# Kernel tuning notes

Measured on AMD Instinct MI355X. Metric: run time of the kernel, lower is better.

## Reference

```python
import jax, jax.numpy as jnp
import numpy as np

N_NODES = 30000
IN_DIM = 8
HIDDEN = 64
HEADS1 = 8
OUT_DIM = 8
NEG_SLOPE = 0.2


def _glorot(key, shape):
    fan_in, fan_out = shape[0], shape[-1]
    lim = jnp.sqrt(6.0 / (fan_in + fan_out))
    return jax.random.uniform(key, shape, jnp.float32, -lim, lim)


def setup_inputs() -> dict:
    key = jax.random.key(0)
    ks = jax.random.split(key, 12)
    x = jax.random.normal(ks[0], (N_NODES, IN_DIM), jnp.float32)
    edge_index = jax.random.randint(ks[1], (2, 300000), 0, N_NODES, jnp.int32)
    # layer 1: in=8, out=HIDDEN per head, 8 heads, concat
    W1l = _glorot(ks[2], (IN_DIM, HEADS1 * HIDDEN))
    W1r = _glorot(ks[3], (IN_DIM, HEADS1 * HIDDEN))
    a1 = _glorot(ks[4], (HEADS1, HIDDEN))
    b1 = jnp.zeros((HEADS1 * HIDDEN,), jnp.float32)
    # layer 2: in=HEADS1*HIDDEN, out=OUT_DIM, 1 head
    W2l = _glorot(ks[5], (HEADS1 * HIDDEN, OUT_DIM))
    W2r = _glorot(ks[6], (HEADS1 * HIDDEN, OUT_DIM))
    a2 = _glorot(ks[7], (1, OUT_DIM))
    b2 = jnp.zeros((OUT_DIM,), jnp.float32)
    return {"x": x, "edge_index": edge_index, "W1l": W1l, "W1r": W1r,
            "a1": a1, "b1": b1, "W2l": W2l, "W2r": W2r, "a2": a2, "b2": b2}


def gatv2_layer(x, src, dst, Wl, Wr, att, bias, heads, out_ch):
    n = x.shape[0]
    xl = (x @ Wl).reshape(n, heads, out_ch)   # messages (source side)
    xr = (x @ Wr).reshape(n, heads, out_ch)   # target side
    h = jax.nn.leaky_relu(xl[src] + xr[dst], NEG_SLOPE)   # [E,H,C]
    e = jnp.einsum('ehc,hc->eh', h, att)                  # [E,H]
    # segment softmax over incoming edges per destination node
    m = jax.ops.segment_max(e, dst, num_segments=n)
    p = jnp.exp(e - m[dst])
    denom = jax.ops.segment_sum(p, dst, num_segments=n)
    alpha = p / denom[dst]                                # [E,H]
    out = jax.ops.segment_sum(alpha[..., None] * xl[src], dst, num_segments=n)
    return out.reshape(n, heads * out_ch) + bias


def reference(x, edge_index, W1l, W1r, a1, b1, W2l, W2r, a2, b2):
    n = x.shape[0]
    loops = jnp.arange(n, dtype=edge_index.dtype)
    src = jnp.concatenate([edge_index[0], loops])  # add_self_loops=True (PyG default)
    dst = jnp.concatenate([edge_index[1], loops])
    h = gatv2_layer(x, src, dst, W1l, W1r, a1, b1, HEADS1, HIDDEN)
    h = jax.nn.relu(h)
    out = gatv2_layer(h, src, dst, W2l, W2r, a2, b2, 1, OUT_DIM)
    return out
```

## Files before the change

### kernel.cpp

```cpp
#include <hip/hip_runtime.h>
#include <math.h>

#define N_NODES   30000
#define N_EDGE    300000
#define N_EDGE_T  330000
#define HEADS     8
#define HIDDEN    64
#define IN_DIM    8
#define OUT_DIM   8
#define NEG_SLOPE 0.2f

#define PIN_V(v) asm volatile("" : "+v"(v))

#define DPP_ADDF(x, ctrl)                                                     \
    x += __int_as_float(__builtin_amdgcn_update_dpp(                          \
            0, __float_as_int(x), (ctrl), 0xF, 0xF, true))
#define RED16(x) do { DPP_ADDF(x, 0xB1); DPP_ADDF(x, 0x4E);                   \
                      DPP_ADDF(x, 0x141); DPP_ADDF(x, 0x140); } while (0)
#define RED8(x)  do { DPP_ADDF(x, 0xB1); DPP_ADDF(x, 0x4E);                   \
                      DPP_ADDF(x, 0x141); } while (0)


__global__ __launch_bounds__(256) void zero_kernel(int* __restrict__ count) {
    int i = blockIdx.x * 256 + threadIdx.x;
    if (i < N_NODES) count[i] = 0;
}

__global__ __launch_bounds__(256) void count_kernel(const int* __restrict__ ei,
                                                    int* __restrict__ count) {
    int e = blockIdx.x * 256 + threadIdx.x;
    if (e >= N_EDGE_T) return;
    int d = (e < N_EDGE) ? ei[N_EDGE + e] : (e - N_EDGE);
    atomicAdd(&count[d], 1);
}

__global__ __launch_bounds__(1024) void scan_kernel(const int* __restrict__ count,
                                                    int* __restrict__ row_start,
                                                    int* __restrict__ cursor) {
    __shared__ int wsum[16];
    const int tid  = threadIdx.x;
    const int wave = tid >> 6;
    const int lane = tid & 63;
    const int4* c4 = (const int4*)count;
    const int N4 = N_NODES / 4;
    int run = 0;
    for (int r = 0; r < 4; ++r) {
        const int g  = r * 1024 + tid;
        const int i0 = 2 * g;
        const int i1 = 2 * g + 1;
        int4 v0 = make_int4(0,0,0,0), v1 = make_int4(0,0,0,0);
        if (i0 < N4) v0 = c4[i0];
        if (i1 < N4) v1 = c4[i1];
        int s = v0.x + v0.y + v0.z + v0.w + v1.x + v1.y + v1.z + v1.w;
        int sc = s;
        #pragma unroll
        for (int off = 1; off < 64; off <<= 1) {
            int t = __shfl_up(sc, off, 64);
            if (lane >= off) sc += t;
        }
        if (lane == 63) wsum[wave] = sc;
        __syncthreads();
        if (tid < 16) {
            int w = wsum[tid];
            #pragma unroll
            for (int off = 1; off < 16; off <<= 1) {
                int t = __shfl_up(w, off, 64);
                if (tid >= off) w += t;
            }
            wsum[tid] = w;
        }
        __syncthreads();
        const int woff = (wave > 0) ? wsum[wave - 1] : 0;
        int e0 = run + woff + (sc - s);
        int4 ex0, ex1;
        ex0.x = e0;           ex0.y = ex0.x + v0.x;
        ex0.z = ex0.y + v0.y; ex0.w = ex0.z + v0.z;
        int e4 = ex0.w + v0.w;
        ex1.x = e4;           ex1.y = ex1.x + v1.x;
        ex1.z = ex1.y + v1.y; ex1.w = ex1.z + v1.z;
        if (i0 < N4) { ((int4*)row_start)[i0] = ex0; ((int4*)cursor)[i0] = ex0; }
        if (i1 < N4) { ((int4*)row_start)[i1] = ex1; ((int4*)cursor)[i1] = ex1; }
        const int tot = wsum[15];
        __syncthreads();
        run += tot;
    }
    if (tid == 0) row_start[N_NODES] = run;
}

__global__ __launch_bounds__(256) void scatter_kernel(const int* __restrict__ ei,
                                                      int* __restrict__ cursor,
                                                      int* __restrict__ edge_src) {
    int e = blockIdx.x * 256 + threadIdx.x;
    if (e >= N_EDGE_T) return;
    int s, d;
    if (e < N_EDGE) { s = ei[e]; d = ei[N_EDGE + e]; }
    else            { s = d = e - N_EDGE; }
    int pos = atomicAdd(&cursor[d], 1);
    edge_src[pos] = s;
}


__device__ __forceinline__ float4 ld_row4(const float* __restrict__ x, int s, int o) {
    return *(const float4*)(x + s * IN_DIM + o);
}

__global__ void __launch_bounds__(128, 3)
layer1_kernel(
    const float* __restrict__ x,
    const float* __restrict__ W1l, const float* __restrict__ W1r,
    const float* __restrict__ a1,  const float* __restrict__ b1,
    const float* __restrict__ W2l, const float* __restrict__ W2r,
    const int* __restrict__ row_start, const int* __restrict__ edge_src,
    float* __restrict__ xl2, float* __restrict__ xr2)
{
    const int d    = blockIdx.x;
    const int tid  = threadIdx.x;
    const int head = tid >> 4;
    const int c4   = tid & 15;
    const int colb = head * HIDDEN + c4 * 4;

    int vz; asm("v_mov_b32 %0, 0" : "=v"(vz));
    const int* __restrict__ es = edge_src + vz;

    float wl[IN_DIM][4], av[4];
    #pragma unroll
    for (int k = 0; k < IN_DIM; ++k) {
        const float4 l4 = *(const float4*)&W1l[k * 512 + colb];
        wl[k][0] = l4.x; wl[k][1] = l4.y; wl[k][2] = l4.z; wl[k][3] = l4.w;
    }
    { const float4 a4 = *(const float4*)&a1[colb];
      av[0] = a4.x; av[1] = a4.y; av[2] = a4.z; av[3] = a4.w; }

    float xr[4] = {0.f, 0.f, 0.f, 0.f};
    #pragma unroll
    for (int k = 0; k < IN_DIM; ++k) {
        const float4 r4 = *(const float4*)&W1r[k * 512 + colb];
        const float xv = x[d * IN_DIM + k];
        xr[0] = fmaf(xv, r4.x, xr[0]); xr[1] = fmaf(xv, r4.y, xr[1]);
        xr[2] = fmaf(xv, r4.z, xr[2]); xr[3] = fmaf(xv, r4.w, xr[3]);
    }

    #pragma unroll
    for (int k = 0; k < IN_DIM; ++k) {
        PIN_V(wl[k][0]); PIN_V(wl[k][1]); PIN_V(wl[k][2]); PIN_V(wl[k][3]);
    }
    PIN_V(av[0]); PIN_V(av[1]); PIN_V(av[2]); PIN_V(av[3]);
    PIN_V(xr[0]); PIN_V(xr[1]); PIN_V(xr[2]); PIN_V(xr[3]);

    const int rs = row_start[d];
    const int re = row_start[d + 1];

    float denom  = 0.f;
    float acc[4] = {0.f, 0.f, 0.f, 0.f};

    auto pair2 = [&](float4 a0, float4 a1_, float4 b0, float4 b1_,
                     bool va, bool vb) {
        const float ra[IN_DIM] = {a0.x, a0.y, a0.z, a0.w, a1_.x, a1_.y, a1_.z, a1_.w};
        const float rb[IN_DIM] = {b0.x, b0.y, b0.z, b0.w, b1_.x, b1_.y, b1_.z, b1_.w};
        float v0a = xr[0], v1a = xr[1], v2a = xr[2], v3a = xr[3];
        float v0b = xr[0], v1b = xr[1], v2b = xr[2], v3b = xr[3];
        #pragma unroll
        for (int k = 0; k < IN_DIM; ++k) {
            const float xa = ra[k], xb = rb[k];
            v0a = fmaf(xa, wl[k][0], v0a); v0b = fmaf(xb, wl[k][0], v0b);
            v1a = fmaf(xa, wl[k][1], v1a); v1b = fmaf(xb, wl[k][1], v1b);
            v2a = fmaf(xa, wl[k][2], v2a); v2b = fmaf(xb, wl[k][2], v2b);
            v3a = fmaf(xa, wl[k][3], v3a); v3b = fmaf(xb, wl[k][3], v3b);
        }
        float ta, tb, ea, eb;
        ta = fmaxf(v0a, NEG_SLOPE * v0a); ea = av[0] * ta;
        tb = fmaxf(v0b, NEG_SLOPE * v0b); eb = av[0] * tb;
        ta = fmaxf(v1a, NEG_SLOPE * v1a); ea = fmaf(av[1], ta, ea);
        tb = fmaxf(v1b, NEG_SLOPE * v1b); eb = fmaf(av[1], tb, eb);
        ta = fmaxf(v2a, NEG_SLOPE * v2a); ea = fmaf(av[2], ta, ea);
        tb = fmaxf(v2b, NEG_SLOPE * v2b); eb = fmaf(av[2], tb, eb);
        ta = fmaxf(v3a, NEG_SLOPE * v3a); ea = fmaf(av[3], ta, ea);
        tb = fmaxf(v3b, NEG_SLOPE * v3b); eb = fmaf(av[3], tb, eb);
        RED16(ea); RED16(eb);
        float pa = va ? __expf(ea) : 0.f;
        float pb = vb ? __expf(eb) : 0.f;
        denom += pa + pb;
        acc[0] = fmaf(pb, v0b, fmaf(pa, v0a, acc[0]));
        acc[1] = fmaf(pb, v1b, fmaf(pa, v1a, acc[1]));
        acc[2] = fmaf(pb, v2b, fmaf(pa, v2a, acc[2]));
        acc[3] = fmaf(pb, v3b, fmaf(pa, v3a, acc[3]));
    };

    float4 rA0, rA1, rB0, rB1, rC0, rC1, rD0, rD1;
    {
        int e1 = (rs + 1 < re) ? rs + 1 : re - 1;
        int e2 = (rs + 2 < re) ? rs + 2 : re - 1;
        int e3 = (rs + 3 < re) ? rs + 3 : re - 1;
        int s0 = es[rs], s1 = es[e1], s2 = es[e2], s3 = es[e3];
        rA0 = ld_row4(x, s0, 0); rA1 = ld_row4(x, s0, 4);
        rB0 = ld_row4(x, s1, 0); rB1 = ld_row4(x, s1, 4);
        rC0 = ld_row4(x, s2, 0); rC1 = ld_row4(x, s2, 4);
        rD0 = ld_row4(x, s3, 0); rD1 = ld_row4(x, s3, 4);
    }

    int base = rs;
    for (;;) {
        const int  nbase = base + 4;
        const bool more  = nbase < re;

        int ns0 = 0, ns1 = 0, ns2 = 0, ns3 = 0;
        if (more) {
            int f1 = (nbase + 1 < re) ? nbase + 1 : re - 1;
            int f2 = (nbase + 2 < re) ? nbase + 2 : re - 1;
            int f3 = (nbase + 3 < re) ? nbase + 3 : re - 1;
            ns0 = es[nbase]; ns1 = es[f1]; ns2 = es[f2]; ns3 = es[f3];
        }

        pair2(rA0, rA1, rB0, rB1, true, base + 1 < re);

        float4 nA0, nA1, nB0, nB1, nC0, nC1, nD0, nD1;
        if (more) {
            nA0 = ld_row4(x, ns0, 0); nA1 = ld_row4(x, ns0, 4);
            nB0 = ld_row4(x, ns1, 0); nB1 = ld_row4(x, ns1, 4);
            nC0 = ld_row4(x, ns2, 0); nC1 = ld_row4(x, ns2, 4);
            nD0 = ld_row4(x, ns3, 0); nD1 = ld_row4(x, ns3, 4);
        }

        pair2(rC0, rC1, rD0, rD1, base + 2 < re, base + 3 < re);

        if (!more) break;
        base = nbase;
        rA0 = nA0; rA1 = nA1; rB0 = nB0; rB1 = nB1;
        rC0 = nC0; rC1 = nC1; rD0 = nD0; rD1 = nD1;
    }

    const float inv = 1.f / denom;
    const float4 b4 = *(const float4*)&b1[colb];
    float hv[4];
    hv[0] = fmaxf(fmaf(acc[0], inv, b4.x - xr[0]), 0.f);
    hv[1] = fmaxf(fmaf(acc[1], inv, b4.y - xr[1]), 0.f);
    hv[2] = fmaxf(fmaf(acc[2], inv, b4.z - xr[2]), 0.f);
    hv[3] = fmaxf(fmaf(acc[3], inv, b4.w - xr[3]), 0.f);

    float vl[OUT_DIM], vr[OUT_DIM];
    #pragma unroll
    for (int j = 0; j < OUT_DIM; ++j) { vl[j] = 0.f; vr[j] = 0.f; }
    #pragma unroll
    for (int i = 0; i < 4; ++i) {
        const float4 l0 = *(const float4*)&W2l[(colb + i) * OUT_DIM];
        const float4 l1 = *(const float4*)&W2l[(colb + i) * OUT_DIM + 4];
        const float4 r0 = *(const float4*)&W2r[(colb + i) * OUT_DIM];
        const float4 r1 = *(const float4*)&W2r[(colb + i) * OUT_DIM + 4];
        vl[0] = fmaf(hv[i], l0.x, vl[0]); vl[1] = fmaf(hv[i], l0.y, vl[1]);
        vl[2] = fmaf(hv[i], l0.z, vl[2]); vl[3] = fmaf(hv[i], l0.w, vl[3]);
        vl[4] = fmaf(hv[i], l1.x, vl[4]); vl[5] = fmaf(hv[i], l1.y, vl[5]);
        vl[6] = fmaf(hv[i], l1.z, vl[6]); vl[7] = fmaf(hv[i], l1.w, vl[7]);
        vr[0] = fmaf(hv[i], r0.x, vr[0]); vr[1] = fmaf(hv[i], r0.y, vr[1]);
        vr[2] = fmaf(hv[i], r0.z, vr[2]); vr[3] = fmaf(hv[i], r0.w, vr[3]);
        vr[4] = fmaf(hv[i], r1.x, vr[4]); vr[5] = fmaf(hv[i], r1.y, vr[5]);
        vr[6] = fmaf(hv[i], r1.z, vr[6]); vr[7] = fmaf(hv[i], r1.w, vr[7]);
    }
    #pragma unroll
    for (int j = 0; j < OUT_DIM; ++j) { RED16(vl[j]); RED16(vr[j]); }

    __shared__ float psl[HEADS][OUT_DIM];
    __shared__ float psr[HEADS][OUT_DIM];
    if (c4 == 0) {
        #pragma unroll
        for (int j = 0; j < OUT_DIM; ++j) { psl[head][j] = vl[j]; psr[head][j] = vr[j]; }
    }
    __syncthreads();
    if (tid < 16) {
        const int side = tid >> 3, j = tid & 7;
        float s = 0.f;
        if (side == 0) {
            #pragma unroll
            for (int h = 0; h < HEADS; ++h) s += psl[h][j];
            xl2[d * OUT_DIM + j] = s;
        } else {
            #pragma unroll
            for (int h = 0; h < HEADS; ++h) s += psr[h][j];
            xr2[d * OUT_DIM + j] = s;
        }
    }
}


__global__ __launch_bounds__(256) void layer2_kernel(
    const float* __restrict__ xl2, const float* __restrict__ xr2,
    const float* __restrict__ a2,  const float* __restrict__ b2,
    const int* __restrict__ row_start, const int* __restrict__ edge_src,
    float* __restrict__ out)
{
    const int wave = threadIdx.x >> 6;
    const int lane = threadIdx.x & 63;
    const int d = blockIdx.x * 4 + wave;
    if (d >= N_NODES) return;
    const int sub = lane >> 3;
    const int c   = lane & 7;

    const float a_c  = a2[c];
    const float xr_d = xr2[d * OUT_DIM + c];

    const int rs = row_start[d];
    const int re = row_start[d + 1];

    float denom = 0.f, acc = 0.f;

    for (int base = rs; base < re; base += 8) {
        int e = base + sub;
        bool valid = (e < re);
        int s = valid ? edge_src[e] : 0;
        float xls = xl2[s * OUT_DIM + c];
        float v = xls + xr_d;
        float t = fmaxf(v, NEG_SLOPE * v);
        float eh = a_c * t;
        RED8(eh);
        float p = valid ? __expf(eh) : 0.f;
        denom += p;
        acc = fmaf(p, xls, acc);
    }

    denom += __shfl_xor(denom, 8,  64);  acc += __shfl_xor(acc, 8,  64);
    denom += __shfl_xor(denom, 16, 64);  acc += __shfl_xor(acc, 16, 64);
    denom += __shfl_xor(denom, 32, 64);  acc += __shfl_xor(acc, 32, 64);

    if (sub == 0) out[d * OUT_DIM + c] = acc / denom + b2[c];
}


extern "C" void kernel_launch(void* const* d_in, const int* in_sizes, int n_in,
                              void* d_out, int out_size, void* d_ws, size_t ws_size,
                              hipStream_t stream) {
    const float* x   = (const float*)d_in[0];
    const int*   ei  = (const int*)  d_in[1];
    const float* W1l = (const float*)d_in[2];
    const float* W1r = (const float*)d_in[3];
    const float* a1  = (const float*)d_in[4];
    const float* b1  = (const float*)d_in[5];
    const float* W2l = (const float*)d_in[6];
    const float* W2r = (const float*)d_in[7];
    const float* a2  = (const float*)d_in[8];
    const float* b2  = (const float*)d_in[9];
    float* out = (float*)d_out;

    char* ws = (char*)d_ws;
    size_t off = 0;
    auto carve = [&](size_t bytes) { char* p = ws + off; off += (bytes + 255) & ~size_t(255); return p; };
    int*   count     = (int*)  carve(N_NODES * sizeof(int));
    int*   row_start = (int*)  carve((N_NODES + 1) * sizeof(int));
    int*   cursor    = (int*)  carve(N_NODES * sizeof(int));
    int*   edge_src  = (int*)  carve(N_EDGE_T * sizeof(int));
    float* xl2       = (float*)carve(N_NODES * OUT_DIM * sizeof(float));
    float* xr2       = (float*)carve(N_NODES * OUT_DIM * sizeof(float));

    zero_kernel   <<<(N_NODES  + 255) / 256, 256, 0, stream>>>(count);
    count_kernel  <<<(N_EDGE_T + 255) / 256, 256, 0, stream>>>(ei, count);
    scan_kernel   <<<1, 1024, 0, stream>>>(count, row_start, cursor);
    scatter_kernel<<<(N_EDGE_T + 255) / 256, 256, 0, stream>>>(ei, cursor, edge_src);
    layer1_kernel <<<N_NODES, 128, 0, stream>>>(x, W1l, W1r, a1, b1, W2l, W2r,
                                                row_start, edge_src, xl2, xr2);
    layer2_kernel <<<(N_NODES + 3) / 4, 256, 0, stream>>>(xl2, xr2, a2, b2,
                                                          row_start, edge_src, out);
}
```

Baseline: 307.0 us.

## Precompute layer-1 source projection table instead of recomputing per edge

Adds a projection kernel that materialises xl = x @ W1l for all nodes (30000x512 floats), and layer1 now gathers 16-byte slices of this table per edge rather than gathering 32-byte x rows and doing 32 FMAs per edge. This removes per-edge recomputation and frees the registers that held W1l, so the occupancy hint rises from 3 to 4. In exchange it writes and then randomly reads a table of roughly 61 MB, so per-edge gather traffic grows from one 32-byte x row to the full 2 KB table row across the 128 threads, which may not stay in cache.

```diff
diff --git a/kernel.cpp b/kernel.cpp
--- a/kernel.cpp
+++ b/kernel.cpp
@@ -100,14 +100,37 @@
 }
 
 
-__device__ __forceinline__ float4 ld_row4(const float* __restrict__ x, int s, int o) {
-    return *(const float4*)(x + s * IN_DIM + o);
-}
-
-__global__ void __launch_bounds__(128, 3)
+__global__ __launch_bounds__(256) void proj_kernel(
+    const float* __restrict__ x, const float* __restrict__ W1l,
+    float* __restrict__ xl_t)
+{
+    const int t = threadIdx.x;
+    float wl0[IN_DIM], wl1[IN_DIM];
+    #pragma unroll
+    for (int k = 0; k < IN_DIM; ++k) {
+        wl0[k] = W1l[k * 512 + t];
+        wl1[k] = W1l[k * 512 + t + 256];
+    }
+    for (int n = blockIdx.x; n < N_NODES; n += gridDim.x) {
+        float xv[IN_DIM];
+        #pragma unroll
+        for (int k = 0; k < IN_DIM; ++k) xv[k] = x[n * IN_DIM + k];
+        float l0 = 0.f, l1 = 0.f;
+        #pragma unroll
+        for (int k = 0; k < IN_DIM; ++k) {
+            l0 = fmaf(xv[k], wl0[k], l0);
+            l1 = fmaf(xv[k], wl1[k], l1);
+        }
+        xl_t[n * 512 + t]       = l0;
+        xl_t[n * 512 + t + 256] = l1;
+    }
+}
+
+
+__global__ void __launch_bounds__(128, 4)
 layer1_kernel(
     const float* __restrict__ x,
-    const float* __restrict__ W1l, const float* __restrict__ W1r,
+    const float* __restrict__ xl_t, const float* __restrict__ W1r,
     const float* __restrict__ a1,  const float* __restrict__ b1,
     const float* __restrict__ W2l, const float* __restrict__ W2r,
     const int* __restrict__ row_start, const int* __restrict__ edge_src,
@@ -119,33 +142,20 @@
     const int c4   = tid & 15;
     const int colb = head * HIDDEN + c4 * 4;
 
-    int vz; asm("v_mov_b32 %0, 0" : "=v"(vz));
-    const int* __restrict__ es = edge_src + vz;
-
-    float wl[IN_DIM][4], av[4];
-    #pragma unroll
-    for (int k = 0; k < IN_DIM; ++k) {
-        const float4 l4 = *(const float4*)&W1l[k * 512 + colb];
-        wl[k][0] = l4.x; wl[k][1] = l4.y; wl[k][2] = l4.z; wl[k][3] = l4.w;
-    }
+    float av[4];
     { const float4 a4 = *(const float4*)&a1[colb];
       av[0] = a4.x; av[1] = a4.y; av[2] = a4.z; av[3] = a4.w; }
 
-    float xr[4] = {0.f, 0.f, 0.f, 0.f};
+    float xrv[4] = {0.f, 0.f, 0.f, 0.f};
     #pragma unroll
     for (int k = 0; k < IN_DIM; ++k) {
         const float4 r4 = *(const float4*)&W1r[k * 512 + colb];
         const float xv = x[d * IN_DIM + k];
-        xr[0] = fmaf(xv, r4.x, xr[0]); xr[1] = fmaf(xv, r4.y, xr[1]);
-        xr[2] = fmaf(xv, r4.z, xr[2]); xr[3] = fmaf(xv, r4.w, xr[3]);
-    }
-
-    #pragma unroll
-    for (int k = 0; k < IN_DIM; ++k) {
-        PIN_V(wl[k][0]); PIN_V(wl[k][1]); PIN_V(wl[k][2]); PIN_V(wl[k][3]);
+        xrv[0] = fmaf(xv, r4.x, xrv[0]); xrv[1] = fmaf(xv, r4.y, xrv[1]);
+        xrv[2] = fmaf(xv, r4.z, xrv[2]); xrv[3] = fmaf(xv, r4.w, xrv[3]);
     }
     PIN_V(av[0]); PIN_V(av[1]); PIN_V(av[2]); PIN_V(av[3]);
-    PIN_V(xr[0]); PIN_V(xr[1]); PIN_V(xr[2]); PIN_V(xr[3]);
+    PIN_V(xrv[0]); PIN_V(xrv[1]); PIN_V(xrv[2]); PIN_V(xrv[3]);
 
     const int rs = row_start[d];
     const int re = row_start[d + 1];
@@ -153,49 +163,40 @@
     float denom  = 0.f;
     float acc[4] = {0.f, 0.f, 0.f, 0.f};
 
-    auto pair2 = [&](float4 a0, float4 a1_, float4 b0, float4 b1_,
-                     bool va, bool vb) {
-        const float ra[IN_DIM] = {a0.x, a0.y, a0.z, a0.w, a1_.x, a1_.y, a1_.z, a1_.w};
-        const float rb[IN_DIM] = {b0.x, b0.y, b0.z, b0.w, b1_.x, b1_.y, b1_.z, b1_.w};
-        float v0a = xr[0], v1a = xr[1], v2a = xr[2], v3a = xr[3];
-        float v0b = xr[0], v1b = xr[1], v2b = xr[2], v3b = xr[3];
-        #pragma unroll
-        for (int k = 0; k < IN_DIM; ++k) {
-            const float xa = ra[k], xb = rb[k];
-            v0a = fmaf(xa, wl[k][0], v0a); v0b = fmaf(xb, wl[k][0], v0b);
-            v1a = fmaf(xa, wl[k][1], v1a); v1b = fmaf(xb, wl[k][1], v1b);
-            v2a = fmaf(xa, wl[k][2], v2a); v2b = fmaf(xb, wl[k][2], v2b);
-            v3a = fmaf(xa, wl[k][3], v3a); v3b = fmaf(xb, wl[k][3], v3b);
-        }
+    auto ldrow = [&](int s) { return *(const float4*)&xl_t[s * 512 + colb]; };
+
+    auto pair2 = [&](float4 ra, float4 rb, bool va, bool vb) {
+        float q0a = ra.x + xrv[0], q1a = ra.y + xrv[1];
+        float q2a = ra.z + xrv[2], q3a = ra.w + xrv[3];
+        float q0b = rb.x + xrv[0], q1b = rb.y + xrv[1];
+        float q2b = rb.z + xrv[2], q3b = rb.w + xrv[3];
         float ta, tb, ea, eb;
-        ta = fmaxf(v0a, NEG_SLOPE * v0a); ea = av[0] * ta;
-        tb = fmaxf(v0b, NEG_SLOPE * v0b); eb = av[0] * tb;
-        ta = fmaxf(v1a, NEG_SLOPE * v1a); ea = fmaf(av[1], ta, ea);
-        tb = fmaxf(v1b, NEG_SLOPE * v1b); eb = fmaf(av[1], tb, eb);
-        ta = fmaxf(v2a, NEG_SLOPE * v2a); ea = fmaf(av[2], ta, ea);
-        tb = fmaxf(v2b, NEG_SLOPE * v2b); eb = fmaf(av[2], tb, eb);
-        ta = fmaxf(v3a, NEG_SLOPE * v3a); ea = fmaf(av[3], ta, ea);
-        tb = fmaxf(v3b, NEG_SLOPE * v3b); eb = fmaf(av[3], tb, eb);
+        ta = fmaxf(q0a, NEG_SLOPE * q0a); ea = av[0] * ta;
+        tb = fmaxf(q0b, NEG_SLOPE * q0b); eb = av[0] * tb;
+        ta = fmaxf(q1a, NEG_SLOPE * q1a); ea = fmaf(av[1], ta, ea);
+        tb = fmaxf(q1b, NEG_SLOPE * q1b); eb = fmaf(av[1], tb, eb);
+        ta = fmaxf(q2a, NEG_SLOPE * q2a); ea = fmaf(av[2], ta, ea);
+        tb = fmaxf(q2b, NEG_SLOPE * q2b); eb = fmaf(av[2], tb, eb);
+        ta = fmaxf(q3a, NEG_SLOPE * q3a); ea = fmaf(av[3], ta, ea);
+        tb = fmaxf(q3b, NEG_SLOPE * q3b); eb = fmaf(av[3], tb, eb);
         RED16(ea); RED16(eb);
         float pa = va ? __expf(ea) : 0.f;
         float pb = vb ? __expf(eb) : 0.f;
         denom += pa + pb;
-        acc[0] = fmaf(pb, v0b, fmaf(pa, v0a, acc[0]));
-        acc[1] = fmaf(pb, v1b, fmaf(pa, v1a, acc[1]));
-        acc[2] = fmaf(pb, v2b, fmaf(pa, v2a, acc[2]));
-        acc[3] = fmaf(pb, v3b, fmaf(pa, v3a, acc[3]));
+        acc[0] = fmaf(pb, rb.x, fmaf(pa, ra.x, acc[0]));
+        acc[1] = fmaf(pb, rb.y, fmaf(pa, ra.y, acc[1]));
+        acc[2] = fmaf(pb, rb.z, fmaf(pa, ra.z, acc[2]));
+        acc[3] = fmaf(pb, rb.w, fmaf(pa, ra.w, acc[3]));
     };
 
-    float4 rA0, rA1, rB0, rB1, rC0, rC1, rD0, rD1;
+    float4 rA, rB, rC, rD;
     {
         int e1 = (rs + 1 < re) ? rs + 1 : re - 1;
         int e2 = (rs + 2 < re) ? rs + 2 : re - 1;
         int e3 = (rs + 3 < re) ? rs + 3 : re - 1;
-        int s0 = es[rs], s1 = es[e1], s2 = es[e2], s3 = es[e3];
-        rA0 = ld_row4(x, s0, 0); rA1 = ld_row4(x, s0, 4);
-        rB0 = ld_row4(x, s1, 0); rB1 = ld_row4(x, s1, 4);
-        rC0 = ld_row4(x, s2, 0); rC1 = ld_row4(x, s2, 4);
-        rD0 = ld_row4(x, s3, 0); rD1 = ld_row4(x, s3, 4);
+        int s0 = edge_src[rs], s1 = edge_src[e1];
+        int s2 = edge_src[e2], s3 = edge_src[e3];
+        rA = ldrow(s0); rB = ldrow(s1); rC = ldrow(s2); rD = ldrow(s3);
     }
 
     int base = rs;
@@ -208,34 +209,31 @@
             int f1 = (nbase + 1 < re) ? nbase + 1 : re - 1;
             int f2 = (nbase + 2 < re) ? nbase + 2 : re - 1;
             int f3 = (nbase + 3 < re) ? nbase + 3 : re - 1;
-            ns0 = es[nbase]; ns1 = es[f1]; ns2 = es[f2]; ns3 = es[f3];
-        }
-
-        pair2(rA0, rA1, rB0, rB1, true, base + 1 < re);
-
-        float4 nA0, nA1, nB0, nB1, nC0, nC1, nD0, nD1;
+            ns0 = edge_src[nbase]; ns1 = edge_src[f1];
+            ns2 = edge_src[f2];    ns3 = edge_src[f3];
+        }
+
+        pair2(rA, rB, true, base + 1 < re);
+
+        float4 nA, nB, nC, nD;
         if (more) {
-            nA0 = ld_row4(x, ns0, 0); nA1 = ld_row4(x, ns0, 4);
-            nB0 = ld_row4(x, ns1, 0); nB1 = ld_row4(x, ns1, 4);
-            nC0 = ld_row4(x, ns2, 0); nC1 = ld_row4(x, ns2, 4);
-            nD0 = ld_row4(x, ns3, 0); nD1 = ld_row4(x, ns3, 4);
-        }
-
-        pair2(rC0, rC1, rD0, rD1, base + 2 < re, base + 3 < re);
+            nA = ldrow(ns0); nB = ldrow(ns1); nC = ldrow(ns2); nD = ldrow(ns3);
+        }
+
+        pair2(rC, rD, base + 2 < re, base + 3 < re);
 
         if (!more) break;
         base = nbase;
-        rA0 = nA0; rA1 = nA1; rB0 = nB0; rB1 = nB1;
-        rC0 = nC0; rC1 = nC1; rD0 = nD0; rD1 = nD1;
+        rA = nA; rB = nB; rC = nC; rD = nD;
     }
 
     const float inv = 1.f / denom;
     const float4 b4 = *(const float4*)&b1[colb];
     float hv[4];
-    hv[0] = fmaxf(fmaf(acc[0], inv, b4.x - xr[0]), 0.f);
-    hv[1] = fmaxf(fmaf(acc[1], inv, b4.y - xr[1]), 0.f);
-    hv[2] = fmaxf(fmaf(acc[2], inv, b4.z - xr[2]), 0.f);
-    hv[3] = fmaxf(fmaf(acc[3], inv, b4.w - xr[3]), 0.f);
+    hv[0] = fmaxf(fmaf(acc[0], inv, b4.x), 0.f);
+    hv[1] = fmaxf(fmaf(acc[1], inv, b4.y), 0.f);
+    hv[2] = fmaxf(fmaf(acc[2], inv, b4.z), 0.f);
+    hv[3] = fmaxf(fmaf(acc[3], inv, b4.w), 0.f);
 
     float vl[OUT_DIM], vr[OUT_DIM];
     #pragma unroll
@@ -348,12 +346,14 @@
     int*   edge_src  = (int*)  carve(N_EDGE_T * sizeof(int));
     float* xl2       = (float*)carve(N_NODES * OUT_DIM * sizeof(float));
     float* xr2       = (float*)carve(N_NODES * OUT_DIM * sizeof(float));
-
+    float* xl_t      = (float*)carve((size_t)N_NODES * 512 * sizeof(float));
+
+    proj_kernel   <<<1024, 256, 0, stream>>>(x, W1l, xl_t);
     zero_kernel   <<<(N_NODES  + 255) / 256, 256, 0, stream>>>(count);
     count_kernel  <<<(N_EDGE_T + 255) / 256, 256, 0, stream>>>(ei, count);
     scan_kernel   <<<1, 1024, 0, stream>>>(count, row_start, cursor);
     scatter_kernel<<<(N_EDGE_T + 255) / 256, 256, 0, stream>>>(ei, cursor, edge_src);
-    layer1_kernel <<<N_NODES, 128, 0, stream>>>(x, W1l, W1r, a1, b1, W2l, W2r,
+    layer1_kernel <<<N_NODES, 128, 0, stream>>>(x, xl_t, W1r, a1, b1, W2l, W2r,
                                                 row_start, edge_src, xl2, xr2);
     layer2_kernel <<<(N_NODES + 3) / 4, 256, 0, stream>>>(xl2, xr2, a2, b2,
                                                           row_start, edge_src, out);
```

Result: no change. 302.5 us (-1.5%).
